# Optimization experiments

Hardware: AMD Instinct MI355X
Metric: run time of the kernel (lower is better)

Reference implementation:

```python
import jax, jax.numpy as jnp
import numpy as np
import math

B, H, W, DM = 4, 64, 64, 96
DS, DCONV, EXPAND = 16, 3, 2
DI = EXPAND * DM
DTR = math.ceil(DM / 16)
K = 4
HID = 4 * DI


def layernorm(x, g, b, eps=1e-5):
    m = x.mean(-1, keepdims=True)
    v = ((x - m) ** 2).mean(-1, keepdims=True)
    return (x - m) / jnp.sqrt(v + eps) * g + b


def dwconv(x, w, b=None):
    # x: (B,C,H,W), w: (C,1,kh,kw) depthwise, odd kernel => SAME padding == k//2
    out = jax.lax.conv_general_dilated(x, w, (1, 1), 'SAME',
                                       feature_group_count=x.shape[1],
                                       dimension_numbers=('NCHW', 'OIHW', 'NCHW'))
    if b is not None:
        out = out + b[None, :, None, None]
    return out


def ss2d_core(xc, x_proj_w, dt_projs_w, dt_projs_b, A_logs, Ds):
    # xc: (b, d_inner, h, w) -> (b, d_inner, L) summed over 4 scan directions
    b, c, h, w = xc.shape
    L = h * w
    x_hw = xc.reshape(b, c, L)
    x_wh = xc.transpose(0, 1, 3, 2).reshape(b, c, L)
    xs = jnp.stack([x_hw, x_wh], axis=1)                 # (b,2,c,L)
    xs = jnp.concatenate([xs, jnp.flip(xs, -1)], axis=1)  # (b,4,c,L)
    x_dbl = jnp.einsum('bkdl,kcd->bkcl', xs, x_proj_w)
    dts, Bs, Cs = jnp.split(x_dbl, [DTR, DTR + DS], axis=2)
    dts = jnp.einsum('bkrl,kdr->bkdl', dts, dt_projs_w)
    delta = jax.nn.softplus(dts + dt_projs_b[None, :, :, None])  # (b,K,c,L)
    A = -jnp.exp(A_logs).reshape(K, c, DS)                       # (K,c,n)

    def step(hst, inp):
        x_t, d_t, B_t, C_t = inp  # (b,K,c),(b,K,c),(b,K,n),(b,K,n)
        dA = jnp.exp(d_t[..., None] * A)                       # (b,K,c,n)
        hst = hst * dA + (d_t * x_t)[..., None] * B_t[:, :, None, :]
        y = jnp.einsum('bkdn,bkn->bkd', hst, C_t)
        return hst, y

    seq = (jnp.moveaxis(xs, -1, 0), jnp.moveaxis(delta, -1, 0),
           jnp.moveaxis(Bs, -1, 0), jnp.moveaxis(Cs, -1, 0))
    h0 = jnp.zeros((b, K, c, DS), xc.dtype)
    _, ys = jax.lax.scan(step, h0, seq)          # (L,b,K,c)
    ys = jnp.moveaxis(ys, 0, -1)                 # (b,K,c,L)
    ys = ys + Ds.reshape(K, c)[None, :, :, None] * xs
    y1 = ys[:, 0]
    inv = jnp.flip(ys[:, 2:4], -1)
    y2 = inv[:, 0]
    wh = ys[:, 1].reshape(b, c, w, h).swapaxes(2, 3).reshape(b, c, L)
    invwh = inv[:, 1].reshape(b, c, w, h).swapaxes(2, 3).reshape(b, c, L)
    return y1 + y2 + wh + invwh


def msffn(y, in_w, in_b, dw1, dw3, dw5, ln_g, ln_b, out_w, out_b):
    hcl = jax.nn.silu(y @ in_w.T + in_b)          # (b,h,w,HID)
    hc = hcl.transpose(0, 3, 1, 2)
    hc = hc + dwconv(hc, dw1) + dwconv(hc, dw3) + dwconv(hc, dw5)
    hn = layernorm(hc.transpose(0, 2, 3, 1), ln_g, ln_b)
    return hn @ out_w.T + out_b


def setup_inputs() -> dict:
    key = jax.random.key(0)
    ks = jax.random.split(key, 16)
    dt_init_std = DTR ** -0.5
    dt = jnp.exp(jax.random.uniform(ks[0], (K, DI)) * (math.log(0.1) - math.log(0.001)) + math.log(0.001))
    dt = jnp.clip(dt, 1e-4, None)
    inv_dt = dt + jnp.log(-jnp.expm1(-dt))          # softplus-inverse init for dt bias
    A_logs = jnp.tile(jnp.log(jnp.arange(1, DS + 1, dtype=jnp.float32))[None, :], (K * DI, 1))
    r = lambda i, sh, s: jax.random.normal(ks[i], sh, jnp.float32) * s
    return {
        'x': r(1, (B, H, W, DM), 1.0),
        'in_proj_w': r(2, (2 * DI, DM), DM ** -0.5),
        'conv_w': r(3, (DI, 1, DCONV, DCONV), 0.2),
        'conv_b': jnp.zeros((DI,), jnp.float32),
        'x_proj_w': r(4, (K, DTR + 2 * DS, DI), DI ** -0.5),
        'dt_projs_w': jax.random.uniform(ks[5], (K, DI, DTR), minval=-dt_init_std, maxval=dt_init_std),
        'dt_projs_b': inv_dt,
        'A_logs': A_logs,
        'Ds': jnp.ones((K * DI,), jnp.float32),
        'out_norm_g': jnp.ones((DI,), jnp.float32),
        'out_norm_b': jnp.zeros((DI,), jnp.float32),
        'out_proj_w': r(6, (DM, DI), DI ** -0.5),
        'ffn_in_w': r(7, (HID, DI), DI ** -0.5),
        'ffn_in_b': jnp.zeros((HID,), jnp.float32),
        'ffn_dw1': r(8, (HID, 1, 1, 1), 0.3),
        'ffn_dw3': r(9, (HID, 1, 3, 3), 0.2),
        'ffn_dw5': r(10, (HID, 1, 5, 5), 0.1),
        'ffn_ln_g': jnp.ones((HID,), jnp.float32),
        'ffn_ln_b': jnp.zeros((HID,), jnp.float32),
        'ffn_out_w': r(11, (DM, HID), HID ** -0.5),
        'ffn_out_b': jnp.zeros((DM,), jnp.float32),
        'skip_scale': jnp.ones((1,), jnp.float32),
    }


def reference(x, in_proj_w, conv_w, conv_b, x_proj_w, dt_projs_w, dt_projs_b, A_logs, Ds,
              out_norm_g, out_norm_b, out_proj_w, ffn_in_w, ffn_in_b, ffn_dw1, ffn_dw3,
              ffn_dw5, ffn_ln_g, ffn_ln_b, ffn_out_w, ffn_out_b, skip_scale):
    b, h, w, _ = x.shape
    xz = x @ in_proj_w.T                          # (b,h,w,2*DI)
    xi, z = jnp.split(xz, 2, axis=-1)
    xc = jax.nn.silu(dwconv(xi.transpose(0, 3, 1, 2), conv_w, conv_b))  # (b,DI,h,w)
    y = ss2d_core(xc, x_proj_w, dt_projs_w, dt_projs_b, A_logs, Ds)     # (b,DI,L)
    y = y.swapaxes(1, 2).reshape(b, h, w, DI)
    y = layernorm(y, out_norm_g, out_norm_b)
    y = y * jax.nn.silu(z)
    out = y @ out_proj_w.T
    ffn = msffn(y, ffn_in_w, ffn_in_b, ffn_dw1, ffn_dw3, ffn_dw5,
                ffn_ln_g, ffn_ln_b, ffn_out_w, ffn_out_b)
    return out + skip_scale * ffn
```

## Files before the change

kernel.cpp:

```cpp
#include <hip/hip_runtime.h>
#include <hip/hip_bf16.h>

constexpr int BB = 4, HH = 64, WW = 64, DMv = 96;
constexpr int DSn = 16, DIv = 192, DTRv = 6, KKv = 4, HIDv = 768;
constexpr int LL = 4096;
constexpr int NC = 32, CHK = LL / NC;
constexpr int NR = BB * LL;
constexpr int XDS = 40;

constexpr size_t S_xi   = (size_t)BB * LL * DIv;
constexpr size_t S_xdbl = (size_t)BB * KKv * LL * XDS;
constexpr size_t S_big  = (size_t)BB * KKv * LL * DIv;
constexpr size_t S_sp   = (size_t)BB * KKv * NC * DIv * DSn;

typedef __attribute__((ext_vector_type(8))) short short8;
typedef __attribute__((ext_vector_type(4))) short short4v;
typedef __attribute__((ext_vector_type(4))) float floatx4;

__device__ __forceinline__ float sigf(float x) { return 1.f / (1.f + __expf(-x)); }
__device__ __forceinline__ float softp(float x) {
  return (x > 20.f) ? x : __logf(1.f + __expf(x));
}
__device__ __forceinline__ short bfbits(float v) {
  __hip_bfloat16 h = __float2bfloat16(v);
  return *(short*)&h;
}
__device__ __forceinline__ float ex2(float x) {
#if __has_builtin(__builtin_amdgcn_exp2f)
  return __builtin_amdgcn_exp2f(x);
#else
  return exp2f(x);
#endif
}

__device__ __forceinline__ int lmap(int k, int l) {
  int lr = (k & 2) ? (LL - 1 - l) : l;
  return (k & 1) ? (((lr & 63) << 6) | (lr >> 6)) : lr;
}

__global__ void k_wprep(const float* __restrict__ fiw, const float* __restrict__ opw,
                        const float* __restrict__ fow, const float* __restrict__ in_w,
                        const float* __restrict__ xpw, const float* __restrict__ x,
                        float* __restrict__ wt, float* __restrict__ xt,
                        short* __restrict__ fiwP, short* __restrict__ opwP,
                        short* __restrict__ fowP, short* __restrict__ wcatP) {
  int bx = blockIdx.x, t = threadIdx.x;
  __shared__ float smbuf[32 * 65];
  if (bx < 36) {
    int r0 = (bx / 3) * 32, c0 = (bx % 3) * 32;
    float (*tile)[33] = (float(*)[33])smbuf;
    int tc = t & 31, tr = t >> 5;
#pragma unroll
    for (int i = 0; i < 4; ++i)
      tile[tr + i * 8][tc] = in_w[(size_t)(r0 + tr + i * 8) * 96 + c0 + tc];
    __syncthreads();
#pragma unroll
    for (int i = 0; i < 4; ++i)
      wt[(size_t)(c0 + tr + i * 8) * 384 + r0 + tc] = tile[tc][tr + i * 8];
    return;
  }
  if (bx < 804) {
    int i4 = bx - 36;
    int r0 = (i4 / 3) * 64, k0 = (i4 % 3) * 32;
    float (*tile)[65] = (float(*)[65])smbuf;
#pragma unroll
    for (int ii = 0; ii < 8; ++ii) {
      int i = (t >> 5) + ii * 8, j = t & 31;
      tile[j][i] = x[(size_t)(r0 + i) * 96 + k0 + j];
    }
    __syncthreads();
#pragma unroll
    for (int jj = 0; jj < 8; ++jj) {
      int j = (t >> 6) + jj * 4, i = t & 63;
      xt[(size_t)(k0 + j) * NR + r0 + i] = tile[j][i];
    }
    return;
  }
  int lane = t & 63, ln16 = lane & 15, qd = lane >> 4;
  if (bx < 876) {
    int f = (bx - 804) * 4 + (t >> 6);
    int kt = f / 48, ntg = f % 48;
    int n = ntg * 16 + ln16;
#pragma unroll
    for (int j = 0; j < 8; ++j) {
      int k = kt * 32 + qd * 8 + j;
      fiwP[(size_t)f * 512 + lane * 8 + j] = bfbits(fiw[(size_t)n * DIv + k]);
    }
    return;
  }
  if (bx < 894) {
    int u = (bx - 876) * 4 + (t >> 6);
    int f = u >> 1, part = u & 1;
    int kt = f / 6, ntg = f % 6;
    int n = ntg * 16 + ln16;
#pragma unroll
    for (int j = 0; j < 8; ++j) {
      int k = kt * 32 + qd * 8 + j;
      float w = opw[(size_t)n * DIv + k];
      __hip_bfloat16 h = __float2bfloat16(w);
      float v = part ? (w - (float)h) : w;
      opwP[((size_t)(part * 36 + f)) * 512 + lane * 8 + j] = bfbits(v);
    }
    return;
  }
  if (bx < 966) {
    int u = (bx - 894) * 4 + (t >> 6);
    int f = u >> 1, part = u & 1;
    int kt = f / 6, ntg = f % 6;
    int n = ntg * 16 + ln16;
#pragma unroll
    for (int j = 0; j < 8; ++j) {
      int k = kt * 32 + qd * 8 + j;
      float w = fow[(size_t)n * HIDv + k];
      __hip_bfloat16 h = __float2bfloat16(w);
      float v = part ? (w - (float)h) : w;
      fowP[((size_t)(part * 144 + f)) * 512 + lane * 8 + j] = bfbits(v);
    }
    return;
  }
  {
    int u = (bx - 966) * 4 + (t >> 6);
    int p = u / 60, r = u % 60;
    int part = r / 30, r2 = r % 30;
    int kt = r2 / 5, g = r2 % 5;
    int n = g * 16 + ln16;
#pragma unroll
    for (int j = 0; j < 8; ++j) {
      int kd = kt * 32 + qd * 8 + j;
      float w = 0.f;
      if (n < 76) {
        int ksel = ((n >= 38) ? 2 : 0) + p;
        int cc = (n >= 38) ? n - 38 : n;
        w = xpw[(size_t)(ksel * 38 + cc) * DIv + kd];
      }
      __hip_bfloat16 h = __float2bfloat16(w);
      float v = part ? (w - (float)h) : w;
      wcatP[((size_t)(((p * 2 + part) * 6 + kt) * 5 + g)) * 512 + lane * 8 + j] = bfbits(v);
    }
  }
}

__global__ void k_inproj(const float* __restrict__ xt, const float* __restrict__ wt,
                         float* __restrict__ xi, float* __restrict__ z) {
  int t = threadIdx.x;
  int wv = t >> 6, lane = t & 63;
  int rq = blockIdx.x * 256 + wv * 64 + lane;
  int c0 = blockIdx.y * 8;
  const float4* xt4 = (const float4*)xt;
  float4 acc[8];
#pragma unroll
  for (int c = 0; c < 8; ++c) acc[c] = make_float4(0.f, 0.f, 0.f, 0.f);
  for (int k = 0; k < 96; ++k) {
    float4 xv = xt4[(size_t)k * (NR / 4) + rq];
    const float* wr = wt + k * 384 + c0;
#pragma unroll
    for (int c = 0; c < 8; ++c) {
      float w = wr[c];
      acc[c].x += w * xv.x; acc[c].y += w * xv.y;
      acc[c].z += w * xv.z; acc[c].w += w * xv.w;
    }
  }
  float* dst; int cc;
  if (c0 < DIv) { dst = xi; cc = c0; } else { dst = z; cc = c0 - DIv; }
#pragma unroll
  for (int li = 0; li < 4; ++li) {
    size_t row = (size_t)rq * 4 + li;
    float4 v0, v1;
    v0.x = (&acc[0].x)[li]; v0.y = (&acc[1].x)[li];
    v0.z = (&acc[2].x)[li]; v0.w = (&acc[3].x)[li];
    v1.x = (&acc[4].x)[li]; v1.y = (&acc[5].x)[li];
    v1.z = (&acc[6].x)[li]; v1.w = (&acc[7].x)[li];
    float4* o4 = (float4*)(dst + row * DIv + cc);
    o4[0] = v0; o4[1] = v1;
  }
}

constexpr int TW2 = 18;
__global__ void k_dwconv3(const float* __restrict__ xi, const float* __restrict__ cw,
                          const float* __restrict__ cb, float* __restrict__ xc,
                          short* __restrict__ xcBh, short* __restrict__ xcBl) {
  int tile = blockIdx.x;
  int cg = blockIdx.y, b = blockIdx.z;
  int t = threadIdx.x;
  int ti0 = (tile >> 2) * 16, tj0 = (tile & 3) * 16;
  __shared__ float sm[TW2 * TW2 * 32];

  for (int e = t; e < TW2 * TW2 * 32; e += 256) {
    int ec = e & 31;
    int sp = e >> 5;
    int hi = sp / TW2, hj = sp % TW2;
    int gi = ti0 + hi - 1, gj = tj0 + hj - 1;
    float v = 0.f;
    if ((unsigned)gi < (unsigned)HH && (unsigned)gj < (unsigned)WW)
      v = xi[((size_t)b * LL + gi * WW + gj) * DIv + cg * 32 + ec];
    sm[e] = v;
  }

  int c = t & 31, s0 = t >> 5;
  int cglob = cg * 32 + c;
  float wc[9];
#pragma unroll
  for (int j = 0; j < 9; ++j) wc[j] = cw[cglob * 9 + j];
  float bv = cb[cglob];
  __syncthreads();

  float res[32];
  for (int i = 0; i < 32; ++i) {
    int p = s0 + (i << 3);
    int r = p >> 4, q = p & 15;
    float s = bv;
#pragma unroll
    for (int di = 0; di < 3; ++di)
#pragma unroll
      for (int dj = 0; dj < 3; ++dj)
        s += sm[((r + di) * TW2 + (q + dj)) * 32 + c] * wc[di * 3 + dj];
    res[i] = s * sigf(s);
  }
  __syncthreads();
  for (int i = 0; i < 32; ++i) {
    int p = s0 + (i << 3);
    sm[p * 35 + c] = res[i];
  }
  __syncthreads();
  for (int it = 0; it < 32; ++it) {
    int e = it * 256 + t;
    int p = e >> 5, ec = e & 31;
    int l = (ti0 + (p >> 4)) * WW + tj0 + (p & 15);
    float v = sm[p * 35 + ec];
    size_t idx = ((size_t)b * LL + l) * DIv + cg * 32 + ec;
    xc[idx] = v;
    __hip_bfloat16 hh = __float2bfloat16(v);
    xcBh[idx] = *(short*)&hh;
    xcBl[idx] = bfbits(v - (float)hh);
  }
}

__global__ void k_xdblmf(const short* __restrict__ xcBh, const short* __restrict__ xcBl,
                         const short* __restrict__ wcatP, float* __restrict__ xdbl) {
  int t = threadIdx.x;
  int wv = t >> 6, lane = t & 63;
  int ln16 = lane & 15, qd = lane >> 4;
  int pb = blockIdx.y;
  int p = pb >> 2, b = pb & 3;
  int m0 = blockIdx.x * 64 + wv * 16;
  int r = m0 + ln16;
  int l = p ? (((r & 63) << 6) | (r >> 6)) : r;
  const short* ah = xcBh + ((size_t)(b * LL + l)) * DIv + qd * 8;
  const short* al = xcBl + ((size_t)(b * LL + l)) * DIv + qd * 8;
  floatx4 acc[5];
  floatx4 zero4 = {0.f, 0.f, 0.f, 0.f};
#pragma unroll
  for (int g = 0; g < 5; ++g) acc[g] = zero4;
#pragma unroll
  for (int kt = 0; kt < 6; ++kt) {
    short8 Ah = *(const short8*)(ah + kt * 32);
    short8 Al = *(const short8*)(al + kt * 32);
    const short* bh = wcatP + ((size_t)(((p * 2 + 0) * 6 + kt) * 5)) * 512 + lane * 8;
    const short* bl = wcatP + ((size_t)(((p * 2 + 1) * 6 + kt) * 5)) * 512 + lane * 8;
#pragma unroll
    for (int g = 0; g < 5; ++g) {
      short8 Bh = *(const short8*)(bh + (size_t)g * 512);
      short8 Bl = *(const short8*)(bl + (size_t)g * 512);
      acc[g] = __builtin_amdgcn_mfma_f32_16x16x32_bf16(Ah, Bh, acc[g], 0, 0, 0);
      acc[g] = __builtin_amdgcn_mfma_f32_16x16x32_bf16(Al, Bh, acc[g], 0, 0, 0);
      acc[g] = __builtin_amdgcn_mfma_f32_16x16x32_bf16(Ah, Bl, acc[g], 0, 0, 0);
    }
  }
#pragma unroll
  for (int g = 0; g < 5; ++g) {
    int col = g * 16 + ln16;
    if (col < 76) {
#pragma unroll
      for (int rr = 0; rr < 4; ++rr) {
        int rowr = m0 + qd * 4 + rr;
        int kk = (col >= 38) ? (2 + p) : p;
        int cc = (col >= 38) ? col - 38 : col;
        int lpos = (col >= 38) ? (LL - 1 - rowr) : rowr;
        int phys = cc + (cc >= 6 ? 2 : 0);
        size_t ro = (((size_t)(b * KKv + kk)) * LL + lpos) * XDS;
        xdbl[ro + phys] = acc[g][rr];
        if (col == 5) { xdbl[ro + 6] = 0.f; xdbl[ro + 7] = 0.f; }
      }
    }
  }
}

__global__ void k_scan1(const float* __restrict__ xdbl, const float* __restrict__ xc,
                        const float* __restrict__ alogs, const float* __restrict__ dtw,
                        const float* __restrict__ dtb,
                        float* __restrict__ S, float* __restrict__ P) {
  int bx = blockIdx.x;
  int c = bx / 3, dblk = bx % 3;
  int k = blockIdx.y, b = blockIdx.z;
  int t = threadIdx.x, dl = t >> 2, nq = t & 3;
  int d = dblk * 64 + dl;
  __shared__ float xv_s[16][64], bc_s[16][16], dt_s[16][8];
  float A2[4];
#pragma unroll
  for (int j = 0; j < 4; ++j)
    A2[j] = -__expf(alogs[(size_t)(k * DIv + d) * DSn + nq * 4 + j]) * 1.44269504f;
  float DTWr[6];
  float DTBr = dtb[k * DIv + d];
#pragma unroll
  for (int r2 = 0; r2 < 6; ++r2) DTWr[r2] = dtw[(size_t)(k * DIv + d) * 6 + r2];
  size_t bkL = (size_t)(b * KKv + k) * LL;
  const float* xq = xdbl + bkL * XDS;
  const float* xcb = xc + (size_t)b * LL * DIv;
  float h[4] = {0.f, 0.f, 0.f, 0.f}, sA[4] = {0.f, 0.f, 0.f, 0.f};
  int l0 = c * CHK;
  int sr = t >> 4, sq = t & 15;
  float4 xvp, bcp, dtp;
  {
    int lc = lmap(k, l0 + sr);
    xvp = *(const float4*)(xcb + (size_t)lc * DIv + dblk * 64 + sq * 4);
    if (t < 64) bcp = *(const float4*)(xq + (size_t)(l0 + (t >> 2)) * XDS + 8 + (t & 3) * 4);
    if (t < 32) dtp = *(const float4*)(xq + (size_t)(l0 + (t >> 1)) * XDS + (t & 1) * 4);
  }
  for (int tile = 0; tile < CHK / 16; ++tile) {
    *(float4*)&xv_s[sr][sq * 4] = xvp;
    if (t < 64) *(float4*)&bc_s[t >> 2][(t & 3) * 4] = bcp;
    if (t < 32) *(float4*)&dt_s[t >> 1][(t & 1) * 4] = dtp;
    __syncthreads();
    float de_local[4];
#pragma unroll
    for (int jj = 0; jj < 4; ++jj) {
      const float* dr = dt_s[nq * 4 + jj];
      float s = DTBr + dr[0] * DTWr[0] + dr[1] * DTWr[1] + dr[2] * DTWr[2]
                     + dr[3] * DTWr[3] + dr[4] * DTWr[4] + dr[5] * DTWr[5];
      de_local[jj] = softp(s);
    }
    if (tile + 1 < CHK / 16) {
      int ln = l0 + (tile + 1) * 16;
      int lc = lmap(k, ln + sr);
      xvp = *(const float4*)(xcb + (size_t)lc * DIv + dblk * 64 + sq * 4);
      if (t < 64) bcp = *(const float4*)(xq + (size_t)(ln + (t >> 2)) * XDS + 8 + (t & 3) * 4);
      if (t < 32) dtp = *(const float4*)(xq + (size_t)(ln + (t >> 1)) * XDS + (t & 1) * 4);
    }
#pragma unroll
    for (int i2 = 0; i2 < 16; ++i2) {
      float de = __shfl(de_local[i2 & 3], i2 >> 2, 4);
      float xv = xv_s[i2][dl];
      float4 Bv = *(float4*)&bc_s[i2][nq * 4];
      float db = de * xv;
#pragma unroll
      for (int j = 0; j < 4; ++j) {
        float u = de * A2[j];
        sA[j] += u;
        h[j] = h[j] * ex2(u) + db * (&Bv.x)[j];
      }
    }
    __syncthreads();
  }
  size_t o = ((((size_t)(b * KKv + k) * NC + c) * 3 + dblk) * 1024) + (size_t)t * 4;
  float4 hs, ps;
#pragma unroll
  for (int j = 0; j < 4; ++j) { (&hs.x)[j] = h[j]; (&ps.x)[j] = ex2(sA[j]); }
  *(float4*)(S + o) = hs;
  *(float4*)(P + o) = ps;
}

__global__ void k_scan2(float* __restrict__ S, const float* __restrict__ P) {
  int dblk = blockIdx.x, k = blockIdx.y, b = blockIdx.z;
  int t = threadIdx.x;
  size_t base = (((size_t)(b * KKv + k) * NC) * 3 + dblk) * 1024 + (size_t)t * 4;
  float4 h = make_float4(0.f, 0.f, 0.f, 0.f);
  for (int c = 0; c < NC; ++c) {
    size_t o = base + (size_t)c * 3 * 1024;
    float4 s = *(float4*)(S + o), p = *(float4*)(P + o);
    *(float4*)(S + o) = h;
    h.x = s.x + p.x * h.x; h.y = s.y + p.y * h.y;
    h.z = s.z + p.z * h.z; h.w = s.w + p.w * h.w;
  }
}

__global__ void k_scan3(const float* __restrict__ xdbl, const float* __restrict__ xc,
                        const float* __restrict__ alogs, const float* __restrict__ dtw,
                        const float* __restrict__ dtb,
                        const float* __restrict__ Hin, float* __restrict__ ys) {
  int bx = blockIdx.x;
  int c = bx / 3, dblk = bx % 3;
  int k = blockIdx.y, b = blockIdx.z;
  int t = threadIdx.x, dl = t >> 2, nq = t & 3;
  int d = dblk * 64 + dl;
  __shared__ float xv_s[16][64], bc_s[16][32], dt_s[16][8];
  float A2[4];
#pragma unroll
  for (int j = 0; j < 4; ++j)
    A2[j] = -__expf(alogs[(size_t)(k * DIv + d) * DSn + nq * 4 + j]) * 1.44269504f;
  float DTWr[6];
  float DTBr = dtb[k * DIv + d];
#pragma unroll
  for (int r2 = 0; r2 < 6; ++r2) DTWr[r2] = dtw[(size_t)(k * DIv + d) * 6 + r2];
  size_t bkL = (size_t)(b * KKv + k) * LL;
  const float* xq = xdbl + bkL * XDS;
  const float* xcb = xc + (size_t)b * LL * DIv;
  float* yp = ys + bkL * DIv + d;
  size_t o = ((((size_t)(b * KKv + k) * NC + c) * 3 + dblk) * 1024) + (size_t)t * 4;
  float4 h4 = *(const float4*)(Hin + o);
  float h[4] = {h4.x, h4.y, h4.z, h4.w};
  int l0 = c * CHK;
  int sr = t >> 4, sq = t & 15;
  float4 xvp, bcp, dtp;
  {
    int lc = lmap(k, l0 + sr);
    xvp = *(const float4*)(xcb + (size_t)lc * DIv + dblk * 64 + sq * 4);
    if (t < 128) bcp = *(const float4*)(xq + (size_t)(l0 + (t >> 3)) * XDS + 8 + (t & 7) * 4);
    if (t < 32) dtp = *(const float4*)(xq + (size_t)(l0 + (t >> 1)) * XDS + (t & 1) * 4);
  }
  for (int tile = 0; tile < CHK / 16; ++tile) {
    int lt = l0 + tile * 16;
    *(float4*)&xv_s[sr][sq * 4] = xvp;
    if (t < 128) *(float4*)&bc_s[t >> 3][(t & 7) * 4] = bcp;
    if (t < 32) *(float4*)&dt_s[t >> 1][(t & 1) * 4] = dtp;
    __syncthreads();
    float de_local[4];
#pragma unroll
    for (int jj = 0; jj < 4; ++jj) {
      const float* dr = dt_s[nq * 4 + jj];
      float s = DTBr + dr[0] * DTWr[0] + dr[1] * DTWr[1] + dr[2] * DTWr[2]
                     + dr[3] * DTWr[3] + dr[4] * DTWr[4] + dr[5] * DTWr[5];
      de_local[jj] = softp(s);
    }
    if (tile + 1 < CHK / 16) {
      int ln = l0 + (tile + 1) * 16;
      int lc = lmap(k, ln + sr);
      xvp = *(const float4*)(xcb + (size_t)lc * DIv + dblk * 64 + sq * 4);
      if (t < 128) bcp = *(const float4*)(xq + (size_t)(ln + (t >> 3)) * XDS + 8 + (t & 7) * 4);
      if (t < 32) dtp = *(const float4*)(xq + (size_t)(ln + (t >> 1)) * XDS + (t & 1) * 4);
    }
#pragma unroll
    for (int i2 = 0; i2 < 16; ++i2) {
      float de = __shfl(de_local[i2 & 3], i2 >> 2, 4);
      float xv = xv_s[i2][dl];
      float4 Bv = *(float4*)&bc_s[i2][nq * 4];
      float4 Cv = *(float4*)&bc_s[i2][16 + nq * 4];
      float db = de * xv;
      float p = 0.f;
#pragma unroll
      for (int j = 0; j < 4; ++j) {
        h[j] = h[j] * ex2(de * A2[j]) + db * (&Bv.x)[j];
        p += h[j] * (&Cv.x)[j];
      }
      p += __shfl_down(p, 2, 4);
      p += __shfl_down(p, 1, 4);
      if (nq == 0) yp[(size_t)(lt + i2) * DIv] = p;
    }
    __syncthreads();
  }
}

__global__ void k_comlnt(const float* __restrict__ ys, const float* __restrict__ xc,
                         const float* __restrict__ Ds, const float* __restrict__ z,
                         const float* __restrict__ g, const float* __restrict__ be,
                         __hip_bfloat16* __restrict__ ygtB,
                         __hip_bfloat16* __restrict__ ygtBl) {
  int bl0 = blockIdx.x * 32;
  int b = bl0 >> 12, l0 = bl0 & 4095;
  int t = threadIdx.x;
  __shared__ float vbuf[32 * 193];
  __shared__ float m_[32], rs_[32];
  {
    int grp = t >> 6, lane6 = t & 63;
    size_t base = (size_t)b * KKv * LL * DIv;
#pragma unroll
    for (int i8 = 0; i8 < 8; ++i8) {
      int li = grp + i8 * 4;
      int l = l0 + li;
      int lT = ((l & 63) << 6) | (l >> 6);
      const float* r0 = ys + base + (size_t)l * DIv;
      const float* r2 = ys + base + ((size_t)2 * LL + (LL - 1 - l)) * DIv;
      const float* r1 = ys + base + ((size_t)1 * LL + lT) * DIv;
      const float* r3 = ys + base + ((size_t)3 * LL + (LL - 1 - lT)) * DIv;
      const float* xr = xc + ((size_t)b * LL + l) * DIv;
#pragma unroll
      for (int cc = 0; cc < 3; ++cc) {
        int d = lane6 + cc * 64;
        float sd = Ds[d] + Ds[DIv + d] + Ds[2 * DIv + d] + Ds[3 * DIv + d];
        vbuf[li * 193 + d] = r0[d] + r2[d] + r1[d] + r3[d] + sd * xr[d];
      }
    }
  }
  __syncthreads();
  {
    int r = t >> 3, q = t & 7;
    float s = 0.f, qq = 0.f;
#pragma unroll
    for (int j = 0; j < 24; ++j) {
      float v = vbuf[r * 193 + q + j * 8];
      s += v; qq += v * v;
    }
    s += __shfl_down(s, 4, 8); qq += __shfl_down(qq, 4, 8);
    s += __shfl_down(s, 2, 8); qq += __shfl_down(qq, 2, 8);
    s += __shfl_down(s, 1, 8); qq += __shfl_down(qq, 1, 8);
    if (q == 0) {
      float m = s / DIv;
      m_[r] = m;
      rs_[r] = rsqrtf(qq / DIv - m * m + 1e-5f);
    }
  }
  __syncthreads();
  int tc = t & 31, tr = t >> 5;
#pragma unroll
  for (int ch = 0; ch < 6; ++ch) {
    int c0 = ch * 32;
    float gg = g[c0 + tc], bb = be[c0 + tc];
#pragma unroll
    for (int i = 0; i < 4; ++i) {
      int r = tr + i * 8;
      float v = vbuf[r * 193 + c0 + tc];
      float zz = z[(size_t)(bl0 + r) * DIv + c0 + tc];
      float val = (v - m_[r]) * rs_[r] * gg + bb;
      float gated = val * zz * sigf(zz);
      __hip_bfloat16 h = __float2bfloat16(gated);
      ygtB[(size_t)(bl0 + r) * DIv + c0 + tc] = h;
      ygtBl[(size_t)(bl0 + r) * DIv + c0 + tc] = __float2bfloat16(gated - (float)h);
    }
  }
}

__global__ void k_ffnmf(const __hip_bfloat16* __restrict__ ygtB,
                        const short* __restrict__ fiwP,
                        const float* __restrict__ bias, float* __restrict__ hcl) {
  int t = threadIdx.x;
  int wv = t >> 6, lane = t & 63;
  int ln16 = lane & 15, qd = lane >> 4;
  int m0 = blockIdx.x * 64 + wv * 16;
  int n0 = blockIdx.y * 64;
  int ntg0 = n0 >> 4;
  floatx4 acc[4];
  floatx4 zero4 = {0.f, 0.f, 0.f, 0.f};
#pragma unroll
  for (int nt = 0; nt < 4; ++nt) acc[nt] = zero4;
  const short* arow = (const short*)ygtB + (size_t)(m0 + ln16) * DIv + qd * 8;
#pragma unroll
  for (int kt = 0; kt < 6; ++kt) {
    short8 a = *(const short8*)(arow + kt * 32);
    const short* bb = fiwP + ((size_t)(kt * 48 + ntg0) * 64 + lane) * 8;
#pragma unroll
    for (int nt = 0; nt < 4; ++nt) {
      short8 bfr = *(const short8*)(bb + (size_t)nt * 512);
      acc[nt] = __builtin_amdgcn_mfma_f32_16x16x32_bf16(a, bfr, acc[nt], 0, 0, 0);
    }
  }
#pragma unroll
  for (int nt = 0; nt < 4; ++nt) {
    int col = n0 + nt * 16 + ln16;
    float bv = bias[col];
#pragma unroll
    for (int r = 0; r < 4; ++r) {
      int row = m0 + qd * 4 + r;
      float s = acc[nt][r] + bv;
      hcl[(size_t)row * HIDv + col] = s * sigf(s);
    }
  }
}

constexpr int TS = 16, CG = 32, TW = TS + 4;
__global__ void k_ffnconv2(const float* __restrict__ hcl, const float* __restrict__ w1,
                           const float* __restrict__ w3, const float* __restrict__ w5,
                           float* __restrict__ hc2) {
  int tile = blockIdx.x;
  int cg = blockIdx.y, b = blockIdx.z;
  int t = threadIdx.x;
  int ti0 = (tile >> 2) * TS, tj0 = (tile & 3) * TS;
  __shared__ float sm[TW * TW * CG];

  for (int e = t; e < TW * TW * CG; e += 256) {
    int ec = e & 31;
    int sp = e >> 5;
    int hi = sp / TW, hj = sp % TW;
    int gi = ti0 + hi - 2, gj = tj0 + hj - 2;
    float v = 0.f;
    if ((unsigned)gi < (unsigned)HH && (unsigned)gj < (unsigned)WW)
      v = hcl[((size_t)b * LL + gi * WW + gj) * HIDv + cg * CG + ec];
    sm[e] = v;
  }

  int c = t & 31;
  int cglob = cg * CG + c;
  float wc[25];
#pragma unroll
  for (int di = 0; di < 5; ++di)
#pragma unroll
    for (int dj = 0; dj < 5; ++dj) {
      float w = w5[cglob * 25 + di * 5 + dj];
      if (di >= 1 && di <= 3 && dj >= 1 && dj <= 3)
        w += w3[cglob * 9 + (di - 1) * 3 + (dj - 1)];
      if (di == 2 && dj == 2) w += 1.f + w1[cglob];
      wc[di * 5 + dj] = w;
    }
  __syncthreads();

  int q2 = t >> 5;
#pragma unroll
  for (int half = 0; half < 2; ++half) {
    int q = q2 + half * 8;
    float win[5][5];
#pragma unroll
    for (int di = 0; di < 4; ++di)
#pragma unroll
      for (int dj = 0; dj < 5; ++dj)
        win[di][dj] = sm[(di * TW + (q + dj)) * CG + c];
#pragma unroll
    for (int r = 0; r < 16; ++r) {
      int slot = (r + 4) % 5;
#pragma unroll
      for (int dj = 0; dj < 5; ++dj)
        win[slot][dj] = sm[(((r + 4) * TW) + (q + dj)) * CG + c];
      float s = 0.f;
#pragma unroll
      for (int di = 0; di < 5; ++di) {
        int wsl = (r + di) % 5;
#pragma unroll
        for (int dj = 0; dj < 5; ++dj)
          s += win[wsl][dj] * wc[di * 5 + dj];
      }
      hc2[((size_t)b * LL + (ti0 + r) * WW + (tj0 + q)) * HIDv + cglob] = s;
    }
  }
}

constexpr int LNROWS = 16, LNPAD = 776;
__global__ void k_ln2b(const float* __restrict__ hc2, const float* __restrict__ g,
                       const float* __restrict__ be,
                       short* __restrict__ hnBh, short* __restrict__ hnBl) {
  int r0 = blockIdx.x * LNROWS;
  int t = threadIdx.x;
  __shared__ float rows[LNROWS * LNPAD];
  __shared__ float m_[LNROWS], rs_[LNROWS];
#pragma unroll
  for (int i = 0; i < 12; ++i) {
    int idx4 = t + i * 256;
    int row = idx4 / 192, c4 = idx4 % 192;
    float4 v = *(const float4*)(hc2 + (size_t)(r0 + row) * HIDv + c4 * 4);
    *(float4*)&rows[row * LNPAD + c4 * 4] = v;
  }
  __syncthreads();
  {
    int r = t >> 4, q = t & 15;
    float s = 0.f, qq = 0.f;
#pragma unroll
    for (int j = 0; j < 48; ++j) {
      float v = rows[r * LNPAD + q + j * 16];
      s += v; qq += v * v;
    }
    s += __shfl_down(s, 8, 16); qq += __shfl_down(qq, 8, 16);
    s += __shfl_down(s, 4, 16); qq += __shfl_down(qq, 4, 16);
    s += __shfl_down(s, 2, 16); qq += __shfl_down(qq, 2, 16);
    s += __shfl_down(s, 1, 16); qq += __shfl_down(qq, 1, 16);
    if (q == 0) {
      float m = s / HIDv;
      m_[r] = m;
      rs_[r] = rsqrtf(qq / HIDv - m * m + 1e-5f);
    }
  }
  __syncthreads();
#pragma unroll
  for (int i = 0; i < 12; ++i) {
    int idx4 = t + i * 256;
    int row = idx4 / 192, c4 = idx4 % 192;
    float4 v = *(const float4*)&rows[row * LNPAD + c4 * 4];
    float4 gv = *(const float4*)(g + c4 * 4);
    float4 bv = *(const float4*)(be + c4 * 4);
    float m = m_[row], rs = rs_[row];
    short4v hh, ll;
#pragma unroll
    for (int j = 0; j < 4; ++j) {
      float val = ((&v.x)[j] - m) * rs * (&gv.x)[j] + (&bv.x)[j];
      __hip_bfloat16 h = __float2bfloat16(val);
      hh[j] = *(short*)&h;
      ll[j] = bfbits(val - (float)h);
    }
    size_t o = (size_t)(r0 + row) * HIDv + c4 * 4;
    *(short4v*)(hnBh + o) = hh;
    *(short4v*)(hnBl + o) = ll;
  }
}

__global__ void k_finalmf(const short* __restrict__ hnBh, const short* __restrict__ hnBl,
                          const short* __restrict__ fowP,
                          const short* __restrict__ ygtBh, const short* __restrict__ ygtBl,
                          const short* __restrict__ opwP,
                          const float* __restrict__ fob, const float* __restrict__ skip,
                          float* __restrict__ dout) {
  int t = threadIdx.x;
  int wv = t >> 6, lane = t & 63;
  int ln16 = lane & 15, qd = lane >> 4;
  int m0 = blockIdx.x * 64 + wv * 16;
  floatx4 accF[6], accO[6];
  floatx4 zero4 = {0.f, 0.f, 0.f, 0.f};
#pragma unroll
  for (int nt = 0; nt < 6; ++nt) { accF[nt] = zero4; accO[nt] = zero4; }
  const short* arh = hnBh + (size_t)(m0 + ln16) * HIDv + qd * 8;
  const short* arl = hnBl + (size_t)(m0 + ln16) * HIDv + qd * 8;
#pragma unroll 2
  for (int kt = 0; kt < 24; ++kt) {
    short8 ah = *(const short8*)(arh + kt * 32);
    short8 al = *(const short8*)(arl + kt * 32);
    const short* bh = fowP + ((size_t)(kt * 6) * 64 + lane) * 8;
    const short* bl = fowP + ((size_t)(144 + kt * 6) * 64 + lane) * 8;
#pragma unroll
    for (int nt = 0; nt < 6; ++nt) {
      short8 bhv = *(const short8*)(bh + (size_t)nt * 512);
      short8 blv = *(const short8*)(bl + (size_t)nt * 512);
      accF[nt] = __builtin_amdgcn_mfma_f32_16x16x32_bf16(ah, bhv, accF[nt], 0, 0, 0);
      accF[nt] = __builtin_amdgcn_mfma_f32_16x16x32_bf16(al, bhv, accF[nt], 0, 0, 0);
      accF[nt] = __builtin_amdgcn_mfma_f32_16x16x32_bf16(ah, blv, accF[nt], 0, 0, 0);
    }
  }
  const short* orh = ygtBh + (size_t)(m0 + ln16) * DIv + qd * 8;
  const short* orl = ygtBl + (size_t)(m0 + ln16) * DIv + qd * 8;
#pragma unroll 2
  for (int kt = 0; kt < 6; ++kt) {
    short8 ah = *(const short8*)(orh + kt * 32);
    short8 al = *(const short8*)(orl + kt * 32);
    const short* bh = opwP + ((size_t)(kt * 6) * 64 + lane) * 8;
    const short* bl = opwP + ((size_t)(36 + kt * 6) * 64 + lane) * 8;
#pragma unroll
    for (int nt = 0; nt < 6; ++nt) {
      short8 bhv = *(const short8*)(bh + (size_t)nt * 512);
      short8 blv = *(const short8*)(bl + (size_t)nt * 512);
      accO[nt] = __builtin_amdgcn_mfma_f32_16x16x32_bf16(ah, bhv, accO[nt], 0, 0, 0);
      accO[nt] = __builtin_amdgcn_mfma_f32_16x16x32_bf16(al, bhv, accO[nt], 0, 0, 0);
      accO[nt] = __builtin_amdgcn_mfma_f32_16x16x32_bf16(ah, blv, accO[nt], 0, 0, 0);
    }
  }
  float sk = skip[0];
#pragma unroll
  for (int nt = 0; nt < 6; ++nt) {
    int col = nt * 16 + ln16;
    float bv = fob[col];
#pragma unroll
    for (int r = 0; r < 4; ++r) {
      int row = m0 + qd * 4 + r;
      dout[(size_t)row * DMv + col] = accO[nt][r] + sk * (accF[nt][r] + bv);
    }
  }
}

extern "C" void kernel_launch(void* const* d_in, const int* in_sizes, int n_in,
                              void* d_out, int out_size, void* d_ws, size_t ws_size,
                              hipStream_t stream) {
  const float* x        = (const float*)d_in[0];
  const float* in_w     = (const float*)d_in[1];
  const float* conv_w   = (const float*)d_in[2];
  const float* conv_b   = (const float*)d_in[3];
  const float* xpw      = (const float*)d_in[4];
  const float* dtw      = (const float*)d_in[5];
  const float* dtb      = (const float*)d_in[6];
  const float* alogs    = (const float*)d_in[7];
  const float* Ds       = (const float*)d_in[8];
  const float* ong      = (const float*)d_in[9];
  const float* onb      = (const float*)d_in[10];
  const float* opw      = (const float*)d_in[11];
  const float* fiw      = (const float*)d_in[12];
  const float* fib      = (const float*)d_in[13];
  const float* dw1      = (const float*)d_in[14];
  const float* dw3      = (const float*)d_in[15];
  const float* dw5      = (const float*)d_in[16];
  const float* flg      = (const float*)d_in[17];
  const float* flb      = (const float*)d_in[18];
  const float* fow      = (const float*)d_in[19];
  const float* fob      = (const float*)d_in[20];
  const float* skip     = (const float*)d_in[21];

  float* ws    = (float*)d_ws;
  float* xi    = ws;
  float* z     = xi + S_xi;
  float* xc    = z + S_xi;
  float* xdbl  = xc + S_xi;
  float* scr   = xdbl + S_xdbl;
  float* ys    = scr + S_big;
  float* wtiny = ys + S_big;
  float* wt    = wtiny;
  __hip_bfloat16* ygtB = (__hip_bfloat16*)(wt + 36864);
  short* fiwP  = (short*)(wt + 36864) + (size_t)NR * DIv;
  short* opwP  = fiwP + 288 * 512;
  short* fowP  = opwP + 2 * 36 * 512;
  short* wcatP = fowP + 2 * 144 * 512;

  float* xt = scr;
  k_wprep<<<996, 256, 0, stream>>>(fiw, opw, fow, in_w, xpw, x,
                                   wt, xt, fiwP, opwP, fowP, wcatP);

  dim3 gip(NR / 1024, 48);
  k_inproj<<<gip, 256, 0, stream>>>(xt, wt, xi, z);

  short* xcBh = (short*)ys;
  short* xcBl = xcBh + (size_t)NR * DIv;
  dim3 gdw(16, DIv / 32, BB);
  k_dwconv3<<<gdw, 256, 0, stream>>>(xi, conv_w, conv_b, xc, xcBh, xcBl);

  dim3 gxd(LL / 64, 8);
  k_xdblmf<<<gxd, 256, 0, stream>>>(xcBh, xcBl, wcatP, xdbl);

  float* Sbuf = scr;
  float* Pbuf = scr + S_sp;
  dim3 gs13(NC * 3, KKv, BB);
  dim3 gs2(3, KKv, BB);
  k_scan1<<<gs13, 256, 0, stream>>>(xdbl, xc, alogs, dtw, dtb, Sbuf, Pbuf);
  k_scan2<<<gs2, 256, 0, stream>>>(Sbuf, Pbuf);
  k_scan3<<<gs13, 256, 0, stream>>>(xdbl, xc, alogs, dtw, dtb, Sbuf, ys);

  __hip_bfloat16* ygtBl = (__hip_bfloat16*)xi;
  k_comlnt<<<NR / 32, 256, 0, stream>>>(ys, xc, Ds, z, ong, onb, ygtB, ygtBl);

  float* hcl = scr;
  dim3 gmf(NR / 64, HIDv / 64);
  k_ffnmf<<<gmf, 256, 0, stream>>>(ygtB, fiwP, fib, hcl);

  float* hc2 = ys;
  dim3 gc(16, HIDv / CG, BB);
  k_ffnconv2<<<gc, 256, 0, stream>>>(hcl, dw1, dw3, dw5, hc2);

  short* hnBh = (short*)scr;
  short* hnBl = hnBh + (size_t)NR * HIDv;
  k_ln2b<<<NR / LNROWS, 256, 0, stream>>>(hc2, flg, flb, hnBh, hnBl);

  k_finalmf<<<NR / 64, 256, 0, stream>>>(hnBh, hnBl, fowP,
                                         (const short*)ygtB, (const short*)ygtBl, opwP,
                                         fob, skip, (float*)d_out);
}
```

Baseline: 426.9 us.

## Double scan chunk count and compute delta cooperatively into shared memory

Raises the number of scan chunks per sequence from 32 to 64, which gives the chunked scan kernels twice as many blocks and halves the serial length per block. In both scan passes the per-step softplus(delta) is now computed once per (timestep, channel) by the whole block and stored in shared memory. Previously each 4-lane group redundantly computed it for its channel and spread it with shuffles. The register prefetch of the next tile is removed and loads are done synchronously each tile, which may expose global-load latency. The carry-propagation pass also gets twice as many sequential steps.

```diff
diff --git a/kernel.cpp b/kernel.cpp
--- a/kernel.cpp
+++ b/kernel.cpp
@@ -4,7 +4,7 @@
 constexpr int BB = 4, HH = 64, WW = 64, DMv = 96;
 constexpr int DSn = 16, DIv = 192, DTRv = 6, KKv = 4, HIDv = 768;
 constexpr int LL = 4096;
-constexpr int NC = 32, CHK = LL / NC;
+constexpr int NC = 64, CHK = LL / NC;
 constexpr int NR = BB * LL;
 constexpr int XDS = 40;
 
@@ -294,51 +294,49 @@
   int k = blockIdx.y, b = blockIdx.z;
   int t = threadIdx.x, dl = t >> 2, nq = t & 3;
   int d = dblk * 64 + dl;
-  __shared__ float xv_s[16][64], bc_s[16][16], dt_s[16][8];
+  __shared__ float de_s[16][64], xv_s[16][64], bc_s[16][16];
   float A2[4];
 #pragma unroll
   for (int j = 0; j < 4; ++j)
     A2[j] = -__expf(alogs[(size_t)(k * DIv + d) * DSn + nq * 4 + j]) * 1.44269504f;
-  float DTWr[6];
-  float DTBr = dtb[k * DIv + d];
-#pragma unroll
-  for (int r2 = 0; r2 < 6; ++r2) DTWr[r2] = dtw[(size_t)(k * DIv + d) * 6 + r2];
+  int derow = t >> 4, dec0 = (t & 15) * 4;
+  float DTW[4][6], DTB[4];
+#pragma unroll
+  for (int jj = 0; jj < 4; ++jj) {
+    int dd = k * DIv + dblk * 64 + dec0 + jj;
+    DTB[jj] = dtb[dd];
+#pragma unroll
+    for (int r2 = 0; r2 < 6; ++r2) DTW[jj][r2] = dtw[(size_t)dd * 6 + r2];
+  }
   size_t bkL = (size_t)(b * KKv + k) * LL;
   const float* xq = xdbl + bkL * XDS;
   const float* xcb = xc + (size_t)b * LL * DIv;
   float h[4] = {0.f, 0.f, 0.f, 0.f}, sA[4] = {0.f, 0.f, 0.f, 0.f};
   int l0 = c * CHK;
-  int sr = t >> 4, sq = t & 15;
-  float4 xvp, bcp, dtp;
-  {
-    int lc = lmap(k, l0 + sr);
-    xvp = *(const float4*)(xcb + (size_t)lc * DIv + dblk * 64 + sq * 4);
-    if (t < 64) bcp = *(const float4*)(xq + (size_t)(l0 + (t >> 2)) * XDS + 8 + (t & 3) * 4);
-    if (t < 32) dtp = *(const float4*)(xq + (size_t)(l0 + (t >> 1)) * XDS + (t & 1) * 4);
-  }
   for (int tile = 0; tile < CHK / 16; ++tile) {
-    *(float4*)&xv_s[sr][sq * 4] = xvp;
-    if (t < 64) *(float4*)&bc_s[t >> 2][(t & 3) * 4] = bcp;
-    if (t < 32) *(float4*)&dt_s[t >> 1][(t & 1) * 4] = dtp;
+    int lt = l0 + tile * 16;
     __syncthreads();
-    float de_local[4];
-#pragma unroll
-    for (int jj = 0; jj < 4; ++jj) {
-      const float* dr = dt_s[nq * 4 + jj];
-      float s = DTBr + dr[0] * DTWr[0] + dr[1] * DTWr[1] + dr[2] * DTWr[2]
-                     + dr[3] * DTWr[3] + dr[4] * DTWr[4] + dr[5] * DTWr[5];
-      de_local[jj] = softp(s);
-    }
-    if (tile + 1 < CHK / 16) {
-      int ln = l0 + (tile + 1) * 16;
-      int lc = lmap(k, ln + sr);
-      xvp = *(const float4*)(xcb + (size_t)lc * DIv + dblk * 64 + sq * 4);
-      if (t < 64) bcp = *(const float4*)(xq + (size_t)(ln + (t >> 2)) * XDS + 8 + (t & 3) * 4);
-      if (t < 32) dtp = *(const float4*)(xq + (size_t)(ln + (t >> 1)) * XDS + (t & 1) * 4);
-    }
+    {
+      int r = t >> 4, q = t & 15;
+      int lc = lmap(k, lt + r);
+      *(float4*)&xv_s[r][q * 4] = *(const float4*)(xcb + (size_t)lc * DIv + dblk * 64 + q * 4);
+      if (t < 64) {
+        int r2 = t >> 2, q2 = t & 3;
+        *(float4*)&bc_s[r2][q2 * 4] = *(const float4*)(xq + (size_t)(lt + r2) * XDS + 8 + q2 * 4);
+      }
+      const float* dtp = xq + (size_t)(lt + derow) * XDS;
+      float d0 = dtp[0], d1 = dtp[1], d2 = dtp[2], d3 = dtp[3], d4 = dtp[4], d5 = dtp[5];
+#pragma unroll
+      for (int jj = 0; jj < 4; ++jj) {
+        float s = DTB[jj] + d0 * DTW[jj][0] + d1 * DTW[jj][1] + d2 * DTW[jj][2]
+                          + d3 * DTW[jj][3] + d4 * DTW[jj][4] + d5 * DTW[jj][5];
+        de_s[derow][dec0 + jj] = softp(s);
+      }
+    }
+    __syncthreads();
 #pragma unroll
     for (int i2 = 0; i2 < 16; ++i2) {
-      float de = __shfl(de_local[i2 & 3], i2 >> 2, 4);
+      float de = de_s[i2][dl];
       float xv = xv_s[i2][dl];
       float4 Bv = *(float4*)&bc_s[i2][nq * 4];
       float db = de * xv;
@@ -349,7 +347,6 @@
         h[j] = h[j] * ex2(u) + db * (&Bv.x)[j];
       }
     }
-    __syncthreads();
   }
   size_t o = ((((size_t)(b * KKv + k) * NC + c) * 3 + dblk) * 1024) + (size_t)t * 4;
   float4 hs, ps;
@@ -382,15 +379,20 @@
   int k = blockIdx.y, b = blockIdx.z;
   int t = threadIdx.x, dl = t >> 2, nq = t & 3;
   int d = dblk * 64 + dl;
-  __shared__ float xv_s[16][64], bc_s[16][32], dt_s[16][8];
+  __shared__ float de_s[16][64], xv_s[16][64], bc_s[16][32];
   float A2[4];
 #pragma unroll
   for (int j = 0; j < 4; ++j)
     A2[j] = -__expf(alogs[(size_t)(k * DIv + d) * DSn + nq * 4 + j]) * 1.44269504f;
-  float DTWr[6];
-  float DTBr = dtb[k * DIv + d];
-#pragma unroll
-  for (int r2 = 0; r2 < 6; ++r2) DTWr[r2] = dtw[(size_t)(k * DIv + d) * 6 + r2];
+  int derow = t >> 4, dec0 = (t & 15) * 4;
+  float DTW[4][6], DTB[4];
+#pragma unroll
+  for (int jj = 0; jj < 4; ++jj) {
+    int dd = k * DIv + dblk * 64 + dec0 + jj;
+    DTB[jj] = dtb[dd];
+#pragma unroll
+    for (int r2 = 0; r2 < 6; ++r2) DTW[jj][r2] = dtw[(size_t)dd * 6 + r2];
+  }
   size_t bkL = (size_t)(b * KKv + k) * LL;
   const float* xq = xdbl + bkL * XDS;
   const float* xcb = xc + (size_t)b * LL * DIv;
@@ -399,38 +401,30 @@
   float4 h4 = *(const float4*)(Hin + o);
   float h[4] = {h4.x, h4.y, h4.z, h4.w};
   int l0 = c * CHK;
-  int sr = t >> 4, sq = t & 15;
-  float4 xvp, bcp, dtp;
-  {
-    int lc = lmap(k, l0 + sr);
-    xvp = *(const float4*)(xcb + (size_t)lc * DIv + dblk * 64 + sq * 4);
-    if (t < 128) bcp = *(const float4*)(xq + (size_t)(l0 + (t >> 3)) * XDS + 8 + (t & 7) * 4);
-    if (t < 32) dtp = *(const float4*)(xq + (size_t)(l0 + (t >> 1)) * XDS + (t & 1) * 4);
-  }
   for (int tile = 0; tile < CHK / 16; ++tile) {
     int lt = l0 + tile * 16;
-    *(float4*)&xv_s[sr][sq * 4] = xvp;
-    if (t < 128) *(float4*)&bc_s[t >> 3][(t & 7) * 4] = bcp;
-    if (t < 32) *(float4*)&dt_s[t >> 1][(t & 1) * 4] = dtp;
     __syncthreads();
-    float de_local[4];
-#pragma unroll
-    for (int jj = 0; jj < 4; ++jj) {
-      const float* dr = dt_s[nq * 4 + jj];
-      float s = DTBr + dr[0] * DTWr[0] + dr[1] * DTWr[1] + dr[2] * DTWr[2]
-                     + dr[3] * DTWr[3] + dr[4] * DTWr[4] + dr[5] * DTWr[5];
-      de_local[jj] = softp(s);
-    }
-    if (tile + 1 < CHK / 16) {
-      int ln = l0 + (tile + 1) * 16;
-      int lc = lmap(k, ln + sr);
-      xvp = *(const float4*)(xcb + (size_t)lc * DIv + dblk * 64 + sq * 4);
-      if (t < 128) bcp = *(const float4*)(xq + (size_t)(ln + (t >> 3)) * XDS + 8 + (t & 7) * 4);
-      if (t < 32) dtp = *(const float4*)(xq + (size_t)(ln + (t >> 1)) * XDS + (t & 1) * 4);
-    }
+    {
+      int r = t >> 4, q = t & 15;
+      int lc = lmap(k, lt + r);
+      *(float4*)&xv_s[r][q * 4] = *(const float4*)(xcb + (size_t)lc * DIv + dblk * 64 + q * 4);
+      if (t < 128) {
+        int r2 = t >> 3, q2 = t & 7;
+        *(float4*)&bc_s[r2][q2 * 4] = *(const float4*)(xq + (size_t)(lt + r2) * XDS + 8 + q2 * 4);
+      }
+      const float* dtp = xq + (size_t)(lt + derow) * XDS;
+      float d0 = dtp[0], d1 = dtp[1], d2 = dtp[2], d3 = dtp[3], d4 = dtp[4], d5 = dtp[5];
+#pragma unroll
+      for (int jj = 0; jj < 4; ++jj) {
+        float s = DTB[jj] + d0 * DTW[jj][0] + d1 * DTW[jj][1] + d2 * DTW[jj][2]
+                          + d3 * DTW[jj][3] + d4 * DTW[jj][4] + d5 * DTW[jj][5];
+        de_s[derow][dec0 + jj] = softp(s);
+      }
+    }
+    __syncthreads();
 #pragma unroll
     for (int i2 = 0; i2 < 16; ++i2) {
-      float de = __shfl(de_local[i2 & 3], i2 >> 2, 4);
+      float de = de_s[i2][dl];
       float xv = xv_s[i2][dl];
       float4 Bv = *(float4*)&bc_s[i2][nq * 4];
       float4 Cv = *(float4*)&bc_s[i2][16 + nq * 4];
@@ -445,7 +439,6 @@
       p += __shfl_down(p, 1, 4);
       if (nq == 0) yp[(size_t)(lt + i2) * DIv] = p;
     }
-    __syncthreads();
   }
 }
 
```

New measurement: 902.6 us. +111.4%, slower.
